# Kernel optimization log

Hardware: AMD Instinct MI355X
Metric: run time of the kernel (lower is better)

The kernel has to match this reference:

```python
import jax, jax.numpy as jnp
import numpy as np

DIM = 1024
NUM_HEADS = 16
HEAD_DIM = DIM // NUM_HEADS
B, N = 4, 2048


def _rope_sin_cos(seq_len, head_dim, dtype=jnp.float32):
    inv_freq = 1.0 / (10000.0 ** (jnp.arange(0, head_dim, 2, dtype=jnp.float32) / head_dim))
    t = jnp.arange(seq_len, dtype=jnp.float32)
    freqs = jnp.einsum('i,j->ij', t, inv_freq)          # [N, head_dim/2]
    emb = jnp.concatenate([freqs, freqs], axis=-1)      # [N, head_dim]
    return jnp.sin(emb).astype(dtype), jnp.cos(emb).astype(dtype)


def _rotate_half(x):
    x1, x2 = jnp.split(x, 2, axis=-1)
    return jnp.concatenate([-x2, x1], axis=-1)


def setup_inputs() -> dict:
    key = jax.random.key(0)
    k1, k2, k3, k4, k5 = jax.random.split(key, 5)
    scale = 0.02
    return {
        'x': jax.random.normal(k1, (B, N, DIM), dtype=jnp.float32),
        'W_qkv': jax.random.normal(k2, (DIM, 3 * DIM), dtype=jnp.float32) * scale,
        'b_qkv': jax.random.normal(k3, (3 * DIM,), dtype=jnp.float32) * scale,
        'W_proj': jax.random.normal(k4, (DIM, DIM), dtype=jnp.float32) * scale,
        'b_proj': jax.random.normal(k5, (DIM,), dtype=jnp.float32) * scale,
    }


def reference(x, W_qkv, b_qkv, W_proj, b_proj):
    Bsz, Nlen, C = x.shape
    H, Dh = NUM_HEADS, HEAD_DIM
    qkv = x @ W_qkv + b_qkv                              # [B, N, 3C]
    q, k, v = jnp.split(qkv, 3, axis=-1)
    # [B, H, N, Dh]
    q = q.reshape(Bsz, Nlen, H, Dh).transpose(0, 2, 1, 3)
    k = k.reshape(Bsz, Nlen, H, Dh).transpose(0, 2, 1, 3)
    v = v.reshape(Bsz, Nlen, H, Dh).transpose(0, 2, 1, 3)
    sin, cos = _rope_sin_cos(Nlen, Dh, x.dtype)          # [N, Dh] each, broadcast
    q = q * cos + _rotate_half(q) * sin
    k = k * cos + _rotate_half(k) * sin
    scale = 1.0 / jnp.sqrt(jnp.asarray(Dh, x.dtype))
    scores = jnp.einsum('bhqd,bhkd->bhqk', q, k) * scale  # [B, H, N, N]
    attn = jax.nn.softmax(scores, axis=-1)
    out = jnp.einsum('bhqk,bhkd->bhqd', attn, v)          # [B, H, N, Dh]
    out = out.transpose(0, 2, 1, 3).reshape(Bsz, Nlen, C)
    return out @ W_proj + b_proj
```

## Files before the change

kernel.cpp:

```cpp
#include <hip/hip_runtime.h>
#include <hip/hip_bf16.h>
#include <math.h>

#define BSZ 4
#define NSEQ 2048
#define CDIM 1024
#define NH 16
#define DH 64
#define KC 64
#define KMAX_STRIDE 32

typedef _Float16 half8_t __attribute__((ext_vector_type(8)));
typedef _Float16 half4_t __attribute__((ext_vector_type(4)));
typedef __fp16 pk2_t __attribute__((ext_vector_type(2)));
typedef __fp16 pk4_t __attribute__((ext_vector_type(4)));
typedef float floatx4 __attribute__((ext_vector_type(4)));

#define GLOBAL_AS(p) ((const __attribute__((address_space(1))) void*)(p))
#define LDS_AS(p)    ((__attribute__((address_space(3))) void*)(p))

__global__ __launch_bounds__(256) void cast_x_kernel(
    const float* __restrict__ src, _Float16* __restrict__ dst) {
  const size_t i = ((size_t)blockIdx.x * 256 + threadIdx.x) * 8;
  float4 a = *(const float4*)(src + i);
  float4 b = *(const float4*)(src + i + 4);
  half8_t h;
  h[0] = (_Float16)a.x; h[1] = (_Float16)a.y; h[2] = (_Float16)a.z; h[3] = (_Float16)a.w;
  h[4] = (_Float16)b.x; h[5] = (_Float16)b.y; h[6] = (_Float16)b.z; h[7] = (_Float16)b.w;
  *(half8_t*)(dst + i) = h;
}

__global__ __launch_bounds__(256) void transpose_cast_kernel(
    const float* __restrict__ src, _Float16* __restrict__ dst, int R, int C) {
  __shared__ float Ls[64][65];
  const int t = threadIdx.x;
  const int r0 = blockIdx.y * 64, c0 = blockIdx.x * 64;
  {
    const int lr = t >> 2, lcg = (t & 3) * 16;
    const float* s = src + (size_t)(r0 + lr) * C + c0 + lcg;
#pragma unroll
    for (int u = 0; u < 4; ++u)
      *(float4*)&Ls[lr][lcg + 4 * u] = *(const float4*)(s + 4 * u);
  }
  __syncthreads();
  const int c = t >> 2, rg = (t & 3) * 16;
  half8_t h0, h1;
#pragma unroll
  for (int u = 0; u < 8; ++u) h0[u] = (_Float16)Ls[rg + u][c];
#pragma unroll
  for (int u = 0; u < 8; ++u) h1[u] = (_Float16)Ls[rg + 8 + u][c];
  _Float16* d = dst + (size_t)(c0 + c) * R + r0 + rg;
  *(half8_t*)d = h0;
  *(half8_t*)(d + 8) = h1;
}

__global__ __launch_bounds__(256) void rope_prep_kernel(
    float2* __restrict__ tbl, unsigned* __restrict__ kmaxu) {
  const int idx = blockIdx.x * 256 + threadIdx.x;
  const int n = idx >> 5, f = idx & 31;
  const float invf = expf(-9.210340371976184f * ((float)f * (1.0f / 32.0f)));
  float s, c;
  sincosf((float)n * invf, &s, &c);
  tbl[idx] = make_float2(c, s);
  if (blockIdx.x == 0)
    for (int i = threadIdx.x; i < 64 * KMAX_STRIDE; i += 256) kmaxu[i] = 0u;
}

__global__ __launch_bounds__(256) void qkv_gemm_kernel(
    const _Float16* __restrict__ xh, const _Float16* __restrict__ Wt,
    const float* __restrict__ bias, const float2* __restrict__ rope,
    _Float16* __restrict__ Qh, _Float16* __restrict__ Kh,
    _Float16* __restrict__ Vh) {
  __shared__ _Float16 As[128 * 64];
  __shared__ _Float16 Bs[128 * 64];
  const int tid = threadIdx.x;
  const int lane = tid & 63, w = tid >> 6;
  const int m = lane & 15, quad = lane >> 4;
  const int wr = (w >> 1) * 64, wc = (w & 1) * 64;
  const int m0 = blockIdx.y * 128;
  const int N0 = blockIdx.x * 128;
  const int sr = lane >> 3, sc = (lane & 7) * 8;

  floatx4 acc[4][4];
#pragma unroll
  for (int i = 0; i < 4; ++i)
#pragma unroll
    for (int j = 0; j < 4; ++j) acc[i][j] = (floatx4){0.f, 0.f, 0.f, 0.f};

  for (int k0 = 0; k0 < CDIM; k0 += 64) {
    __syncthreads();
#pragma unroll
    for (int i = 0; i < 4; ++i) {
      const int row = (w * 4 + i) * 8 + sr;
      __builtin_amdgcn_global_load_lds(
          GLOBAL_AS(xh + (size_t)(m0 + row) * CDIM + k0 + sc),
          LDS_AS(As + (w * 4 + i) * 512), 16, 0, 0);
      __builtin_amdgcn_global_load_lds(
          GLOBAL_AS(Wt + (size_t)(N0 + row) * CDIM + k0 + sc),
          LDS_AS(Bs + (w * 4 + i) * 512), 16, 0, 0);
    }
    __syncthreads();
#pragma unroll
    for (int ks = 0; ks < 2; ++ks) {
      half8_t af[4], bf[4];
#pragma unroll
      for (int mt = 0; mt < 4; ++mt)
        af[mt] = *(half8_t*)(As + (wr + mt * 16 + m) * 64 + ks * 32 + quad * 8);
#pragma unroll
      for (int nt = 0; nt < 4; ++nt)
        bf[nt] = *(half8_t*)(Bs + (wc + nt * 16 + m) * 64 + ks * 32 + quad * 8);
#pragma unroll
      for (int mt = 0; mt < 4; ++mt)
#pragma unroll
        for (int nt = 0; nt < 4; ++nt)
          acc[mt][nt] = __builtin_amdgcn_mfma_f32_16x16x32_f16(
              af[mt], bf[nt], acc[mt][nt], 0, 0, 0);
    }
  }

  const int F0 = N0 + wc;
  const int which = F0 >> 10;
  const int head = (F0 & 1023) >> 6;
  float bv[4];
#pragma unroll
  for (int nt = 0; nt < 4; ++nt) bv[nt] = bias[F0 + nt * 16 + m];

  if (which == 2) {
#pragma unroll
    for (int mt = 0; mt < 4; ++mt)
#pragma unroll
      for (int reg = 0; reg < 4; ++reg) {
        const int gm = m0 + wr + mt * 16 + 4 * quad + reg;
        const int b = gm >> 11, n = gm & 2047;
        const size_t vbase = ((size_t)(b * NH + head) * DH) * NSEQ + n;
#pragma unroll
        for (int nt = 0; nt < 4; ++nt)
          Vh[vbase + (size_t)(nt * 16 + m) * NSEQ] =
              (_Float16)(acc[mt][nt][reg] + bv[nt]);
      }
  } else {
    _Float16* dst = which ? Kh : Qh;
    const float qs = which ? 1.0f : 0.125f * 1.4426950408889634f;
#pragma unroll
    for (int mt = 0; mt < 4; ++mt)
#pragma unroll
      for (int reg = 0; reg < 4; ++reg) {
        const int gm = m0 + wr + mt * 16 + 4 * quad + reg;
        const int b = gm >> 11, n = gm & 2047;
        const float2 csA = rope[n * 32 + m];
        const float2 csB = rope[n * 32 + 16 + m];
        const size_t obase = ((size_t)(b * NH + head) * NSEQ + n) * DH;
#pragma unroll
        for (int nt = 0; nt < 4; ++nt) {
          const float val = acc[mt][nt][reg] + bv[nt];
          const float rot = (nt < 2) ? -(acc[mt][nt + 2][reg] + bv[nt + 2])
                                     :  (acc[mt][nt - 2][reg] + bv[nt - 2]);
          const float sv = (nt & 1) ? csB.y : csA.y;
          const float cv = (nt & 1) ? csB.x : csA.x;
          dst[obase + nt * 16 + m] = (_Float16)((val * cv + rot * sv) * qs);
        }
      }
  }
}

__global__ __launch_bounds__(256) void qk_norms_kernel(
    const _Float16* __restrict__ Qh, const _Float16* __restrict__ Kh,
    float* __restrict__ qn, unsigned* __restrict__ kmaxu) {
  __shared__ float wmax[4];
  const int tid = threadIdx.x;
  const size_t row = (size_t)blockIdx.x * 32 + (tid >> 3);
  const int c = (tid & 7) * 8;
  half8_t q8 = *(const half8_t*)(Qh + row * DH + c);
  half8_t k8 = *(const half8_t*)(Kh + row * DH + c);
  float qs = 0.f, ks = 0.f;
#pragma unroll
  for (int u = 0; u < 8; ++u) {
    const float qv = (float)q8[u], kv = (float)k8[u];
    qs += qv * qv; ks += kv * kv;
  }
  qs += __shfl_xor(qs, 1, 64); ks += __shfl_xor(ks, 1, 64);
  qs += __shfl_xor(qs, 2, 64); ks += __shfl_xor(ks, 2, 64);
  qs += __shfl_xor(qs, 4, 64); ks += __shfl_xor(ks, 4, 64);
  if ((tid & 7) == 0) qn[row] = sqrtf(qs);
  ks = fmaxf(ks, __shfl_xor(ks, 8, 64));
  ks = fmaxf(ks, __shfl_xor(ks, 16, 64));
  ks = fmaxf(ks, __shfl_xor(ks, 32, 64));
  if ((tid & 63) == 0) wmax[tid >> 6] = ks;
  __syncthreads();
  if (tid == 0) {
    const float mx = fmaxf(fmaxf(wmax[0], wmax[1]), fmaxf(wmax[2], wmax[3]));
    atomicMax(&kmaxu[(row >> 11) * KMAX_STRIDE], __float_as_uint(sqrtf(mx)));
  }
}

__global__ __launch_bounds__(512, 8) void attn_kernel(
    const _Float16* __restrict__ Qh, const _Float16* __restrict__ Kh,
    const _Float16* __restrict__ Vh, const float* __restrict__ qn,
    const unsigned* __restrict__ kmaxu, _Float16* __restrict__ AO) {
  __shared__ _Float16 smem[17408];
  float* Os = (float*)smem;
  _Float16* Ks = smem;
  _Float16* Vt = smem + 4608;

  const int tid = threadIdx.x;
  const int lane = tid & 63;
  const int w = tid >> 6;
  const int m = lane & 15;
  const int quad = lane >> 4;

  const int bid = blockIdx.x;
  const int slot = bid & 7, kk = bid >> 3;
  const int bh = slot + 8 * (kk >> 4);
  const int q0 = (kk & 15) * 128;

  const _Float16* Qb = Qh + (size_t)bh * NSEQ * DH;
  const _Float16* Kb = Kh + (size_t)bh * NSEQ * DH;
  const _Float16* Vb = Vh + (size_t)bh * DH * NSEQ;

  const int rA = q0 + w * 16 + m;
  half8_t qfA0 = *(const half8_t*)(Qb + (size_t)rA * DH + quad * 8);
  half8_t qfA1 = *(const half8_t*)(Qb + (size_t)rA * DH + 32 + quad * 8);

  const float kmx = __uint_as_float(kmaxu[bh * KMAX_STRIDE]);
  const float mA = qn[(size_t)bh * NSEQ + rA] * kmx;

  const int skey = tid >> 3, sdg = (tid & 7) * 8;
  const _Float16* ksrc = Kb + (size_t)skey * DH + sdg;
  const _Float16* vsrc = Vb + (size_t)skey * NSEQ + sdg;
  const int koff = skey * 72 + sdg;

  float lA = 0.f;
  floatx4 OA[4];
#pragma unroll
  for (int nb = 0; nb < 4; ++nb) OA[nb] = (floatx4){0.f, 0.f, 0.f, 0.f};
  const pk2_t one2 = {(__fp16)1.f, (__fp16)1.f};

  const int NCK = NSEQ / KC;
  for (int ck = 0; ck < NCK; ++ck) {
    half8_t k8 = *(const half8_t*)ksrc;  ksrc += KC * DH;
    half8_t v8 = *(const half8_t*)vsrc;  vsrc += KC;
    __syncthreads();
    *(half8_t*)(Ks + koff) = k8;
    *(half8_t*)(Vt + koff) = v8;
    __syncthreads();

#pragma unroll
    for (int kt = 0; kt < 4; ++kt) {
      half8_t kf0 = *(half8_t*)(Ks + (kt * 16 + m) * 72 + quad * 8);
      half8_t kf1 = *(half8_t*)(Ks + (kt * 16 + m) * 72 + 32 + quad * 8);
      __builtin_amdgcn_s_setprio(1);
      floatx4 a = (floatx4){-mA, -mA, -mA, -mA};
      a = __builtin_amdgcn_mfma_f32_16x16x32_f16(kf0, qfA0, a, 0, 0, 0);
      a = __builtin_amdgcn_mfma_f32_16x16x32_f16(kf1, qfA1, a, 0, 0, 0);
      __builtin_amdgcn_s_setprio(0);

      pk2_t a01 = __builtin_amdgcn_cvt_pkrtz(__builtin_exp2f(a[0]),
                                             __builtin_exp2f(a[1]));
      pk2_t a23 = __builtin_amdgcn_cvt_pkrtz(__builtin_exp2f(a[2]),
                                             __builtin_exp2f(a[3]));
      lA = __builtin_amdgcn_fdot2(a01, one2, lA, false);
      lA = __builtin_amdgcn_fdot2(a23, one2, lA, false);
      half4_t phA = __builtin_bit_cast(
          half4_t, (pk4_t)__builtin_shufflevector(a01, a23, 0, 1, 2, 3));

      __builtin_amdgcn_s_setprio(1);
#pragma unroll
      for (int nb = 0; nb < 4; ++nb) {
        half4_t vf = *(half4_t*)(Vt + (nb * 16 + m) * 72 + kt * 16 + quad * 4);
        OA[nb] = __builtin_amdgcn_mfma_f32_16x16x16f16(phA, vf, OA[nb], 0, 0, 0);
      }
      __builtin_amdgcn_s_setprio(0);
    }
  }

  lA += __shfl_xor(lA, 16, 64); lA += __shfl_xor(lA, 32, 64);
  float lA4[4];
#pragma unroll
  for (int r = 0; r < 4; ++r) lA4[r] = __shfl(lA, 4 * quad + r, 64);

  const int b = bh >> 4, h = bh & 15;
  const int ql = tid >> 2, dgo = (tid & 3) * 16;
  const int gq = q0 + ql;
  _Float16* dst = AO + ((size_t)(b * NSEQ + gq)) * CDIM + h * DH + dgo;

  __syncthreads();
#pragma unroll
  for (int nb = 0; nb < 4; ++nb)
#pragma unroll
    for (int r = 0; r < 4; ++r)
      Os[(w * 16 + 4 * quad + r) * 68 + nb * 16 + m] = OA[nb][r] * (1.0f / lA4[r]);
  __syncthreads();
#pragma unroll
  for (int u = 0; u < 2; ++u) {
    half8_t o;
#pragma unroll
    for (int v = 0; v < 8; ++v) o[v] = (_Float16)Os[ql * 68 + dgo + u * 8 + v];
    *(half8_t*)(dst + u * 8) = o;
  }
}

__global__ __launch_bounds__(256) void proj_gemm_kernel(
    const _Float16* __restrict__ Ah, const _Float16* __restrict__ Wt,
    const float* __restrict__ bias, float* __restrict__ out) {
  __shared__ _Float16 As[128 * 64];
  __shared__ _Float16 Bs[128 * 64];
  const int tid = threadIdx.x;
  const int lane = tid & 63, w = tid >> 6;
  const int m = lane & 15, quad = lane >> 4;
  const int wr = (w >> 1) * 64, wc = (w & 1) * 64;
  const int m0 = blockIdx.y * 128;
  const int N0 = blockIdx.x * 128;
  const int sr = lane >> 3, sc = (lane & 7) * 8;

  floatx4 acc[4][4];
#pragma unroll
  for (int i = 0; i < 4; ++i)
#pragma unroll
    for (int j = 0; j < 4; ++j) acc[i][j] = (floatx4){0.f, 0.f, 0.f, 0.f};

  for (int k0 = 0; k0 < CDIM; k0 += 64) {
    __syncthreads();
#pragma unroll
    for (int i = 0; i < 4; ++i) {
      const int row = (w * 4 + i) * 8 + sr;
      __builtin_amdgcn_global_load_lds(
          GLOBAL_AS(Ah + (size_t)(m0 + row) * CDIM + k0 + sc),
          LDS_AS(As + (w * 4 + i) * 512), 16, 0, 0);
      __builtin_amdgcn_global_load_lds(
          GLOBAL_AS(Wt + (size_t)(N0 + row) * CDIM + k0 + sc),
          LDS_AS(Bs + (w * 4 + i) * 512), 16, 0, 0);
    }
    __syncthreads();
#pragma unroll
    for (int ks = 0; ks < 2; ++ks) {
      half8_t af[4], bf[4];
#pragma unroll
      for (int mt = 0; mt < 4; ++mt)
        af[mt] = *(half8_t*)(As + (wr + mt * 16 + m) * 64 + ks * 32 + quad * 8);
#pragma unroll
      for (int nt = 0; nt < 4; ++nt)
        bf[nt] = *(half8_t*)(Bs + (wc + nt * 16 + m) * 64 + ks * 32 + quad * 8);
#pragma unroll
      for (int mt = 0; mt < 4; ++mt)
#pragma unroll
        for (int nt = 0; nt < 4; ++nt)
          acc[mt][nt] = __builtin_amdgcn_mfma_f32_16x16x32_f16(
              af[mt], bf[nt], acc[mt][nt], 0, 0, 0);
    }
  }

  const int F0 = N0 + wc;
  float bv[4];
#pragma unroll
  for (int nt = 0; nt < 4; ++nt) bv[nt] = bias[F0 + nt * 16 + m];
#pragma unroll
  for (int mt = 0; mt < 4; ++mt)
#pragma unroll
    for (int reg = 0; reg < 4; ++reg) {
      const int gm = m0 + wr + mt * 16 + 4 * quad + reg;
#pragma unroll
      for (int nt = 0; nt < 4; ++nt)
        out[(size_t)gm * CDIM + F0 + nt * 16 + m] = acc[mt][nt][reg] + bv[nt];
    }
}

extern "C" void kernel_launch(void* const* d_in, const int* in_sizes, int n_in,
                              void* d_out, int out_size, void* d_ws, size_t ws_size,
                              hipStream_t stream) {
  const float* x     = (const float*)d_in[0];
  const float* Wqkv  = (const float*)d_in[1];
  const float* bqkv  = (const float*)d_in[2];
  const float* Wproj = (const float*)d_in[3];
  const float* bproj = (const float*)d_in[4];
  float* out = (float*)d_out;

  const size_t per = (size_t)BSZ * NH * NSEQ * DH;
  _Float16* xh  = (_Float16*)d_ws;
  _Float16* Wt  = xh + per;
  _Float16* Wpt = Wt + (size_t)3072 * 1024;
  _Float16* Qh  = Wpt + (size_t)1024 * 1024;
  _Float16* Kh  = Qh + per;
  _Float16* Vh  = Kh + per;
  _Float16* AOh = Vh + per;
  float*    qnp = (float*)(AOh + per);
  unsigned* kmx = (unsigned*)(qnp + (size_t)64 * NSEQ);
  float2*   ropet = (float2*)(kmx + 64 * KMAX_STRIDE);

  cast_x_kernel<<<4096, 256, 0, stream>>>(x, xh);
  transpose_cast_kernel<<<dim3(48, 16), 256, 0, stream>>>(Wqkv, Wt, 1024, 3072);
  transpose_cast_kernel<<<dim3(16, 16), 256, 0, stream>>>(Wproj, Wpt, 1024, 1024);
  rope_prep_kernel<<<256, 256, 0, stream>>>(ropet, kmx);
  qkv_gemm_kernel<<<dim3(24, 64), 256, 0, stream>>>(xh, Wt, bqkv, ropet, Qh, Kh, Vh);
  qk_norms_kernel<<<4096, 256, 0, stream>>>(Qh, Kh, qnp, kmx);
  attn_kernel<<<1024, 512, 0, stream>>>(Qh, Kh, Vh, qnp, kmx, AOh);
  proj_gemm_kernel<<<dim3(8, 64), 256, 0, stream>>>(AOh, Wpt, bproj, out);
}
```

Baseline: 319.3 us.

## Merge prep kernels into one launch and fuse Q/K norms into QKV GEMM epilogue

Combines the x cast, both weight transpose-casts and the RoPE table/kmax init into a single block-indexed prep kernel. It also computes per-row Q norms and per-head K max norms inside the QKV GEMM epilogue using wave shuffles, so the separate norms kernel no longer re-reads Q and K. This cuts launch count and about 32 MB of fp16 reads, in exchange for extra epilogue registers and shuffles in the GEMM.

```diff
diff --git a/kernel.cpp b/kernel.cpp
--- a/kernel.cpp
+++ b/kernel.cpp
@@ -19,22 +19,47 @@
 #define GLOBAL_AS(p) ((const __attribute__((address_space(1))) void*)(p))
 #define LDS_AS(p)    ((__attribute__((address_space(3))) void*)(p))
 
-__global__ __launch_bounds__(256) void cast_x_kernel(
-    const float* __restrict__ src, _Float16* __restrict__ dst) {
-  const size_t i = ((size_t)blockIdx.x * 256 + threadIdx.x) * 8;
-  float4 a = *(const float4*)(src + i);
-  float4 b = *(const float4*)(src + i + 4);
-  half8_t h;
-  h[0] = (_Float16)a.x; h[1] = (_Float16)a.y; h[2] = (_Float16)a.z; h[3] = (_Float16)a.w;
-  h[4] = (_Float16)b.x; h[5] = (_Float16)b.y; h[6] = (_Float16)b.z; h[7] = (_Float16)b.w;
-  *(half8_t*)(dst + i) = h;
-}
-
-__global__ __launch_bounds__(256) void transpose_cast_kernel(
-    const float* __restrict__ src, _Float16* __restrict__ dst, int R, int C) {
+__global__ __launch_bounds__(256) void prep_kernel(
+    const float* __restrict__ x, const float* __restrict__ Wqkv,
+    const float* __restrict__ Wproj, _Float16* __restrict__ xh,
+    _Float16* __restrict__ Wt, _Float16* __restrict__ Wpt,
+    float2* __restrict__ ropet, unsigned* __restrict__ kmaxu) {
   __shared__ float Ls[64][65];
   const int t = threadIdx.x;
-  const int r0 = blockIdx.y * 64, c0 = blockIdx.x * 64;
+  const int bid = blockIdx.x;
+
+  if (bid < 4096) {
+    const size_t i = ((size_t)bid * 256 + t) * 8;
+    float4 a = *(const float4*)(x + i);
+    float4 b = *(const float4*)(x + i + 4);
+    half8_t h;
+    h[0] = (_Float16)a.x; h[1] = (_Float16)a.y; h[2] = (_Float16)a.z; h[3] = (_Float16)a.w;
+    h[4] = (_Float16)b.x; h[5] = (_Float16)b.y; h[6] = (_Float16)b.z; h[7] = (_Float16)b.w;
+    *(half8_t*)(xh + i) = h;
+    return;
+  }
+  if (bid >= 5120) {
+    const int idx = (bid - 5120) * 256 + t;
+    const int n = idx >> 5, f = idx & 31;
+    const float invf = expf(-9.210340371976184f * ((float)f * (1.0f / 32.0f)));
+    float s, c;
+    sincosf((float)n * invf, &s, &c);
+    ropet[idx] = make_float2(c, s);
+    if (bid == 5120)
+      for (int i2 = t; i2 < 64 * KMAX_STRIDE; i2 += 256) kmaxu[i2] = 0u;
+    return;
+  }
+  const float* src;
+  _Float16* dst;
+  int R, C, bx, by;
+  if (bid < 4864) {
+    src = Wqkv; dst = Wt; R = 1024; C = 3072;
+    bx = (bid - 4096) % 48; by = (bid - 4096) / 48;
+  } else {
+    src = Wproj; dst = Wpt; R = 1024; C = 1024;
+    bx = (bid - 4864) % 16; by = (bid - 4864) / 16;
+  }
+  const int r0 = by * 64, c0 = bx * 64;
   {
     const int lr = t >> 2, lcg = (t & 3) * 16;
     const float* s = src + (size_t)(r0 + lr) * C + c0 + lcg;
@@ -54,23 +79,12 @@
   *(half8_t*)(d + 8) = h1;
 }
 
-__global__ __launch_bounds__(256) void rope_prep_kernel(
-    float2* __restrict__ tbl, unsigned* __restrict__ kmaxu) {
-  const int idx = blockIdx.x * 256 + threadIdx.x;
-  const int n = idx >> 5, f = idx & 31;
-  const float invf = expf(-9.210340371976184f * ((float)f * (1.0f / 32.0f)));
-  float s, c;
-  sincosf((float)n * invf, &s, &c);
-  tbl[idx] = make_float2(c, s);
-  if (blockIdx.x == 0)
-    for (int i = threadIdx.x; i < 64 * KMAX_STRIDE; i += 256) kmaxu[i] = 0u;
-}
-
 __global__ __launch_bounds__(256) void qkv_gemm_kernel(
     const _Float16* __restrict__ xh, const _Float16* __restrict__ Wt,
     const float* __restrict__ bias, const float2* __restrict__ rope,
     _Float16* __restrict__ Qh, _Float16* __restrict__ Kh,
-    _Float16* __restrict__ Vh) {
+    _Float16* __restrict__ Vh, float* __restrict__ qn,
+    unsigned* __restrict__ kmaxu) {
   __shared__ _Float16 As[128 * 64];
   __shared__ _Float16 Bs[128 * 64];
   const int tid = threadIdx.x;
@@ -141,6 +155,11 @@
   } else {
     _Float16* dst = which ? Kh : Qh;
     const float qs = which ? 1.0f : 0.125f * 1.4426950408889634f;
+    float ssum[4][4];
+#pragma unroll
+    for (int mt = 0; mt < 4; ++mt)
+#pragma unroll
+      for (int reg = 0; reg < 4; ++reg) ssum[mt][reg] = 0.f;
 #pragma unroll
     for (int mt = 0; mt < 4; ++mt)
 #pragma unroll
@@ -157,39 +176,48 @@
                                      :  (acc[mt][nt - 2][reg] + bv[nt - 2]);
           const float sv = (nt & 1) ? csB.y : csA.y;
           const float cv = (nt & 1) ? csB.x : csA.x;
-          dst[obase + nt * 16 + m] = (_Float16)((val * cv + rot * sv) * qs);
+          const _Float16 h16 = (_Float16)((val * cv + rot * sv) * qs);
+          dst[obase + nt * 16 + m] = h16;
+          const float vv = (float)h16;
+          ssum[mt][reg] += vv * vv;
         }
       }
-  }
-}
-
-__global__ __launch_bounds__(256) void qk_norms_kernel(
-    const _Float16* __restrict__ Qh, const _Float16* __restrict__ Kh,
-    float* __restrict__ qn, unsigned* __restrict__ kmaxu) {
-  __shared__ float wmax[4];
-  const int tid = threadIdx.x;
-  const size_t row = (size_t)blockIdx.x * 32 + (tid >> 3);
-  const int c = (tid & 7) * 8;
-  half8_t q8 = *(const half8_t*)(Qh + row * DH + c);
-  half8_t k8 = *(const half8_t*)(Kh + row * DH + c);
-  float qs = 0.f, ks = 0.f;
-#pragma unroll
-  for (int u = 0; u < 8; ++u) {
-    const float qv = (float)q8[u], kv = (float)k8[u];
-    qs += qv * qv; ks += kv * kv;
-  }
-  qs += __shfl_xor(qs, 1, 64); ks += __shfl_xor(ks, 1, 64);
-  qs += __shfl_xor(qs, 2, 64); ks += __shfl_xor(ks, 2, 64);
-  qs += __shfl_xor(qs, 4, 64); ks += __shfl_xor(ks, 4, 64);
-  if ((tid & 7) == 0) qn[row] = sqrtf(qs);
-  ks = fmaxf(ks, __shfl_xor(ks, 8, 64));
-  ks = fmaxf(ks, __shfl_xor(ks, 16, 64));
-  ks = fmaxf(ks, __shfl_xor(ks, 32, 64));
-  if ((tid & 63) == 0) wmax[tid >> 6] = ks;
-  __syncthreads();
-  if (tid == 0) {
-    const float mx = fmaxf(fmaxf(wmax[0], wmax[1]), fmaxf(wmax[2], wmax[3]));
-    atomicMax(&kmaxu[(row >> 11) * KMAX_STRIDE], __float_as_uint(sqrtf(mx)));
+#pragma unroll
+    for (int mt = 0; mt < 4; ++mt)
+#pragma unroll
+      for (int reg = 0; reg < 4; ++reg) {
+        float s = ssum[mt][reg];
+        s += __shfl_xor(s, 1, 64);
+        s += __shfl_xor(s, 2, 64);
+        s += __shfl_xor(s, 4, 64);
+        s += __shfl_xor(s, 8, 64);
+        ssum[mt][reg] = s;
+      }
+    if (which == 0) {
+      if (m == 0) {
+#pragma unroll
+        for (int mt = 0; mt < 4; ++mt)
+#pragma unroll
+          for (int reg = 0; reg < 4; ++reg) {
+            const int gm = m0 + wr + mt * 16 + 4 * quad + reg;
+            const int b = gm >> 11, n = gm & 2047;
+            qn[(size_t)(b * NH + head) * NSEQ + n] = sqrtf(ssum[mt][reg]);
+          }
+      }
+    } else {
+      float mx = 0.f;
+#pragma unroll
+      for (int mt = 0; mt < 4; ++mt)
+#pragma unroll
+        for (int reg = 0; reg < 4; ++reg) mx = fmaxf(mx, ssum[mt][reg]);
+      mx = fmaxf(mx, __shfl_xor(mx, 16, 64));
+      mx = fmaxf(mx, __shfl_xor(mx, 32, 64));
+      if (lane == 0) {
+        const int b = m0 >> 11;
+        atomicMax(&kmaxu[(b * NH + head) * KMAX_STRIDE],
+                  __float_as_uint(sqrtf(mx)));
+      }
+    }
   }
 }
 
@@ -386,12 +414,9 @@
   unsigned* kmx = (unsigned*)(qnp + (size_t)64 * NSEQ);
   float2*   ropet = (float2*)(kmx + 64 * KMAX_STRIDE);
 
-  cast_x_kernel<<<4096, 256, 0, stream>>>(x, xh);
-  transpose_cast_kernel<<<dim3(48, 16), 256, 0, stream>>>(Wqkv, Wt, 1024, 3072);
-  transpose_cast_kernel<<<dim3(16, 16), 256, 0, stream>>>(Wproj, Wpt, 1024, 1024);
-  rope_prep_kernel<<<256, 256, 0, stream>>>(ropet, kmx);
-  qkv_gemm_kernel<<<dim3(24, 64), 256, 0, stream>>>(xh, Wt, bqkv, ropet, Qh, Kh, Vh);
-  qk_norms_kernel<<<4096, 256, 0, stream>>>(Qh, Kh, qnp, kmx);
+  prep_kernel<<<5376, 256, 0, stream>>>(x, Wqkv, Wproj, xh, Wt, Wpt, ropet, kmx);
+  qkv_gemm_kernel<<<dim3(24, 64), 256, 0, stream>>>(xh, Wt, bqkv, ropet,
+                                                    Qh, Kh, Vh, qnp, kmx);
   attn_kernel<<<1024, 512, 0, stream>>>(Qh, Kh, Vh, qnp, kmx, AOh);
   proj_gemm_kernel<<<dim3(8, 64), 256, 0, stream>>>(AOh, Wpt, bproj, out);
 }
```

New measurement: 322.1 us. Within noise of the previous version (+0.9%).
